# Performance work log

Hardware: AMD Instinct MI355X
Metric: run time of the kernel (lower is better)

## Reference

```python
import jax, jax.numpy as jnp
from jax import lax
import numpy as np


def gru_last(seq, Wih, Whh, bih, bhh):
    """Run a torch-style GRU over seq [N, T, C] and return only h_T [N, H].

    Gate order matches torch.nn.GRU: (r, z, n);
    n = tanh(W_in x + b_in + r * (W_hn h + b_hn)).
    """
    N = seq.shape[0]
    H = Whh.shape[1]

    def step(h, x_t):
        gi = x_t @ Wih.T + bih          # [N, 3H]
        gh = h @ Whh.T + bhh            # [N, 3H]
        i_r, i_z, i_n = jnp.split(gi, 3, axis=-1)
        h_r, h_z, h_n = jnp.split(gh, 3, axis=-1)
        r = jax.nn.sigmoid(i_r + h_r)
        z = jax.nn.sigmoid(i_z + h_z)
        n = jnp.tanh(i_n + r * h_n)
        h_new = (1.0 - z) * n + z * h
        return h_new, None

    h0 = jnp.zeros((N, H), dtype=seq.dtype)
    hT, _ = lax.scan(step, h0, jnp.swapaxes(seq, 0, 1))  # scan over T
    return hT


def setup_inputs() -> dict:
    key = jax.random.key(0)
    ks = jax.random.split(key, 12)
    B, C, T, Fq, H = 8, 64, 256, 256, 128
    s = 0.05
    return {
        "x": jax.random.normal(ks[0], (B, C, T, Fq), dtype=jnp.float32),
        "Wih_t": jax.random.normal(ks[1], (3 * H, C), dtype=jnp.float32) * s,
        "Whh_t": jax.random.normal(ks[2], (3 * H, H), dtype=jnp.float32) * s,
        "bih_t": jax.random.normal(ks[3], (3 * H,), dtype=jnp.float32) * s,
        "bhh_t": jax.random.normal(ks[4], (3 * H,), dtype=jnp.float32) * s,
        "Wih_f": jax.random.normal(ks[5], (3 * H, C), dtype=jnp.float32) * s,
        "Whh_f": jax.random.normal(ks[6], (3 * H, H), dtype=jnp.float32) * s,
        "bih_f": jax.random.normal(ks[7], (3 * H,), dtype=jnp.float32) * s,
        "bhh_f": jax.random.normal(ks[8], (3 * H,), dtype=jnp.float32) * s,
        "Wp": jax.random.normal(ks[9], (C, H), dtype=jnp.float32) * s,
        "bp": jax.random.normal(ks[10], (C,), dtype=jnp.float32) * s,
    }


def reference(x, Wih_t, Whh_t, bih_t, bhh_t, Wih_f, Whh_f, bih_f, bhh_f, Wp, bp):
    B, C, T, Fq = x.shape
    H = Whh_t.shape[1]

    # time GRU: sequences of length T, one per (batch, freq)
    t_in = jnp.transpose(x, (0, 3, 2, 1)).reshape(B * Fq, T, C)
    h_t = gru_last(t_in, Wih_t, Whh_t, bih_t, bhh_t)          # [B*F, H]
    t_vec = jnp.transpose(h_t.reshape(B, Fq, H), (0, 2, 1))    # [B, H, F]

    # freq GRU: sequences of length F, one per (batch, time)
    f_in = jnp.transpose(x, (0, 2, 3, 1)).reshape(B * T, Fq, C)
    h_f = gru_last(f_in, Wih_f, Whh_f, bih_f, bhh_f)          # [B*T, H]
    f_vec = jnp.transpose(h_f.reshape(B, T, H), (0, 2, 1))    # [B, H, T]

    # t_feat [B,H,F,1] expanded along dim2 to T (requires F == T),
    # f_feat [B,H,T,1] expanded along dim3 to F; fused is constant along F.
    s = t_vec + f_vec                                          # [B, H, T]  (F == T)
    out_t = jnp.einsum("ch,bht->bct", Wp, s) + bp[None, :, None]  # 1x1 conv
    return jnp.broadcast_to(out_t[:, :, :, None], (B, C, T, Fq))
```

## Files before the change

### kernel.cpp

```cpp
#include <hip/hip_runtime.h>

#define B_ 8
#define C_ 64
#define T_ 256
#define F_ 256
#define H_ 128
#define TF_ (T_*F_)

typedef _Float16 half_t;
typedef _Float16 half8 __attribute__((ext_vector_type(8)));
typedef float float4v __attribute__((ext_vector_type(4)));

#if __has_builtin(__builtin_amdgcn_exp2f)
#define EXP2F(x) __builtin_amdgcn_exp2f(x)
#else
static __device__ inline float EXP2F(float x) { float r; asm("v_exp_f32 %0, %1" : "=v"(r) : "v"(x)); return r; }
#endif
#if __has_builtin(__builtin_amdgcn_rcpf)
#define RCPF(x) __builtin_amdgcn_rcpf(x)
#else
static __device__ inline float RCPF(float x) { float r; asm("v_rcp_f32 %0, %1" : "=v"(r) : "v"(x)); return r; }
#endif

#define SGB __builtin_amdgcn_sched_group_barrier

#define NEG_L2E  (-1.4426950408889634f)
#define NEG_2L2E (-2.8853900817779268f)

__global__ __launch_bounds__(256) void k_transpose(const float* __restrict__ x,
                                                   half_t* __restrict__ xt) {
    __shared__ float lds[64 * 65];
    int blk = blockIdx.x;
    int b   = blk >> 10;
    int tf0 = (blk & 1023) << 6;
    int tid = threadIdx.x;
    int s = tid & 15;
    int q = tid >> 4;
    const float* xp = x + (size_t)(b * C_) * TF_ + tf0 + s * 4;
#pragma unroll
    for (int i = 0; i < 4; ++i) {
        int c = q + i * 16;
        float4v v = __builtin_nontemporal_load((const float4v*)(xp + (size_t)c * TF_));
#pragma unroll
        for (int j = 0; j < 4; ++j) lds[(s * 4 + j) * 65 + c] = v[j];
    }
    __syncthreads();
    int row = tid >> 2;
    int c0  = (tid & 3) << 4;
    float v[16];
#pragma unroll
    for (int k = 0; k < 16; ++k) v[k] = lds[row * 65 + c0 + k];
    half8 o0, o1;
#pragma unroll
    for (int k = 0; k < 8; ++k) { o0[k] = (half_t)v[k]; o1[k] = (half_t)v[8 + k]; }
    half_t* op = xt + ((size_t)b * TF_ + tf0 + row) * C_ + c0;
    *(half8*)op       = o0;
    *(half8*)(op + 8) = o1;
}

__device__ inline half8 load_w8s(const float* __restrict__ p, float s) {
    half8 r;
#pragma unroll
    for (int k = 0; k < 8; ++k) r[k] = (half_t)(p[k] * s);
    return r;
}

#define MFMA(a, b, c) __builtin_amdgcn_mfma_f32_16x16x32_f16((a), (b), (c), 0, 0, 0)

__global__ __launch_bounds__(512, 2) void k_gru(
    const half_t* __restrict__ xt,
    const float* __restrict__ Wih_t, const float* __restrict__ Whh_t,
    const float* __restrict__ bih_t, const float* __restrict__ bhh_t,
    const float* __restrict__ Wih_f, const float* __restrict__ Whh_f,
    const float* __restrict__ bih_f, const float* __restrict__ bhh_f,
    float* __restrict__ h_t_out, float* __restrict__ h_f_out) {
    __shared__ half_t hbuf0[16 * 136];
    __shared__ half_t hbuf1[16 * 136];

    int tid  = threadIdx.x;
    int w    = tid >> 6;
    int lane = tid & 63;
    int nidx = lane & 15;
    int quad = lane >> 4;

    int bi  = blockIdx.x;
    bool isf = bi >= 128;
    int lbi = bi & 127;
    int b   = lbi >> 4;
    int g16 = (lbi & 15) << 4;

    const float* Wih = isf ? Wih_f : Wih_t;
    const float* Whh = isf ? Whh_f : Whh_t;
    const float* bih = isf ? bih_f : bih_t;
    const float* bhh = isf ? bhh_f : bhh_t;
    float* hout      = isf ? h_f_out : h_t_out;

    size_t Sm = isf ? (size_t)(F_ * C_) : (size_t)C_;
    size_t Ss = isf ? (size_t)C_ : (size_t)(F_ * C_);
    size_t abase = (size_t)b * TF_ * C_ + (size_t)g16 * Sm;

    int gr = w * 16 + nidx;
    int gz = gr + 128;
    int gn = gr + 256;
    int ko = quad * 8;

    half8 wir0 = load_w8s(Wih + gr * 64 + ko,      NEG_L2E);
    half8 wir1 = load_w8s(Wih + gr * 64 + 32 + ko, NEG_L2E);
    half8 wiz0 = load_w8s(Wih + gz * 64 + ko,      NEG_L2E);
    half8 wiz1 = load_w8s(Wih + gz * 64 + 32 + ko, NEG_L2E);
    half8 win0 = load_w8s(Wih + gn * 64 + ko,      NEG_2L2E);
    half8 win1 = load_w8s(Wih + gn * 64 + 32 + ko, NEG_2L2E);
    half8 whr[4], whz[4], whn[4];
#pragma unroll
    for (int kt = 0; kt < 4; ++kt) {
        whr[kt] = load_w8s(Whh + gr * 128 + kt * 32 + ko, NEG_L2E);
        whz[kt] = load_w8s(Whh + gz * 128 + kt * 32 + ko, NEG_L2E);
        whn[kt] = load_w8s(Whh + gn * 128 + kt * 32 + ko, NEG_2L2E);
    }
    float br  = NEG_L2E  * (bih[gr] + bhh[gr]);
    float bz  = NEG_L2E  * (bih[gz] + bhh[gz]);
    float bin = NEG_2L2E * bih[gn];
    float bhn = NEG_2L2E * bhh[gn];
    float4v brv  = {br, br, br, br};
    float4v bzv  = {bz, bz, bz, bz};
    float4v bnv  = {bin, bin, bin, bin};
    float4v bhnv = {bhn, bhn, bhn, bhn};

    for (int idx = tid; idx < 16 * 136; idx += 512) hbuf0[idx] = (half_t)0.f;
    float h_old[4] = {0.f, 0.f, 0.f, 0.f};

    const half_t* ap = xt + abase + (size_t)nidx * Sm + ko;
    half8 xA0 = *(const half8*)ap;
    half8 xA1 = *(const half8*)(ap + 32);
    ap += Ss;
    half8 xB0 = *(const half8*)ap;
    half8 xB1 = *(const half8*)(ap + 32);
    ap += Ss;

    float4v xrE = MFMA(xA0, wir0, brv); xrE = MFMA(xA1, wir1, xrE);
    float4v xzE = MFMA(xA0, wiz0, bzv); xzE = MFMA(xA1, wiz1, xzE);
    float4v xnE = MFMA(xA0, win0, bnv); xnE = MFMA(xA1, win1, xnE);
    float4v xrO = {0.f, 0.f, 0.f, 0.f};
    float4v xzO = {0.f, 0.f, 0.f, 0.f};
    float4v xnO = {0.f, 0.f, 0.f, 0.f};
    __syncthreads();

#define GRU_STEP(RBUF, WBUF, XR, XZ, XN, XRn, XZn, XNn, XC0, XC1, XP0, XP1)     \
    {                                                                           \
        const half_t* hrow = (RBUF) + nidx * 136 + ko;                          \
        half8 ha0 = *(const half8*)(hrow);                                      \
        half8 ha1 = *(const half8*)(hrow + 32);                                 \
        half8 ha2 = *(const half8*)(hrow + 64);                                 \
        half8 ha3 = *(const half8*)(hrow + 96);                                 \
        XP0 = *(const half8*)ap;                                                \
        XP1 = *(const half8*)(ap + 32);                                         \
        ap += Ss;                                                               \
        XR = MFMA(ha0, whr[0], XR); XR = MFMA(ha1, whr[1], XR);                 \
        XR = MFMA(ha2, whr[2], XR); XR = MFMA(ha3, whr[3], XR);                 \
        XZ = MFMA(ha0, whz[0], XZ); XZ = MFMA(ha1, whz[1], XZ);                 \
        XZ = MFMA(ha2, whz[2], XZ); XZ = MFMA(ha3, whz[3], XZ);                 \
        float4v hnv = MFMA(ha0, whn[0], bhnv);                                  \
        hnv = MFMA(ha1, whn[1], hnv);                                           \
        float rr[4], Ez[4];                                                     \
        _Pragma("unroll")                                                       \
        for (int rg = 0; rg < 4; ++rg) rr[rg] = RCPF(1.f + EXP2F(XR[rg]));      \
        hnv = MFMA(ha2, whn[2], hnv);                                           \
        hnv = MFMA(ha3, whn[3], hnv);                                           \
        _Pragma("unroll")                                                       \
        for (int rg = 0; rg < 4; ++rg) Ez[rg] = EXP2F(XZ[rg]);                  \
                                          \
        XRn = MFMA(XC0, wir0, brv); XRn = MFMA(XC1, wir1, XRn);                 \
        XZn = MFMA(XC0, wiz0, bzv); XZn = MFMA(XC1, wiz1, XZn);                 \
        XNn = MFMA(XC0, win0, bnv); XNn = MFMA(XC1, win1, XNn);                 \
        _Pragma("unroll")                                                       \
        for (int rg = 0; rg < 4; ++rg) {                                        \
            float np  = XN[rg] + rr[rg] * hnv[rg];                              \
            float En  = EXP2F(np);                                              \
            float u   = __builtin_fmaf(h_old[rg], En, h_old[rg]);               \
            float t2  = u + Ez[rg];                                             \
            float num = __builtin_fmaf(-En, Ez[rg], t2);                        \
            float den = (1.f + En) * (1.f + Ez[rg]);                            \
            float h   = num * RCPF(den);                                        \
            h_old[rg] = h;                                                      \
            (WBUF)[(quad * 4 + rg) * 136 + w * 16 + nidx] = (half_t)h;          \
        }                                                                       \
                                     \
        SGB(0x100, 4, 0);                    \
        SGB(0x020, 2, 0);                    \
        SGB(0x008, 8, 0);                    \
        SGB(0x002, 12, 0);                   \
        SGB(0x008, 4, 0);                    \
        SGB(0x002, 8, 0);                    \
        SGB(0x008, 6, 0);                    \
        SGB(0x002, 48, 0);                   \
        SGB(0x200, 4, 0);                    \
        __syncthreads();                                                        \
    }

    for (int it = 0; it < 128; ++it) {
        GRU_STEP(hbuf0, hbuf1, xrE, xzE, xnE, xrO, xzO, xnO, xB0, xB1, xA0, xA1)
        GRU_STEP(hbuf1, hbuf0, xrO, xzO, xnO, xrE, xzE, xnE, xA0, xA1, xB0, xB1)
    }
#undef GRU_STEP

    int srow = (b << 8) + g16;
#pragma unroll
    for (int rg = 0; rg < 4; ++rg) {
        hout[(size_t)(srow + quad * 4 + rg) * H_ + w * 16 + nidx] = h_old[rg];
    }
}

__global__ __launch_bounds__(256) void k_out(const float* __restrict__ h_t,
                                             const float* __restrict__ h_f,
                                             const float* __restrict__ Wp,
                                             const float* __restrict__ bp,
                                             float* __restrict__ out) {
    __shared__ float sv[128];
    __shared__ float part[4][64];
    __shared__ float orow[64];
    int blk = blockIdx.x;
    int b = blk >> 8;
    int i = blk & 255;
    int tid = threadIdx.x;
    size_t hoff = ((size_t)(b * 256 + i)) * 128;
    if (tid < 128) sv[tid] = h_t[hoff + tid] + h_f[hoff + tid];
    __syncthreads();
    int c = tid & 63;
    int q = tid >> 6;
    float p = 0.f;
    const float* wp = Wp + c * 128 + q * 32;
#pragma unroll
    for (int k = 0; k < 32; ++k) p += wp[k] * sv[q * 32 + k];
    part[q][c] = p;
    __syncthreads();
    if (tid < 64) orow[tid] = part[0][tid] + part[1][tid] + part[2][tid] + part[3][tid] + bp[tid];
    __syncthreads();
    int wv   = tid >> 6;
    int lane = tid & 63;
#pragma unroll
    for (int itr = 0; itr < 16; ++itr) {
        int cc = itr * 4 + wv;
        float v = orow[cc];
        float4v vv = {v, v, v, v};
        __builtin_nontemporal_store(vv, (float4v*)(out + (((size_t)(b * 64 + cc)) * 256 + i) * 256 + lane * 4));
    }
}

extern "C" void kernel_launch(void* const* d_in, const int* in_sizes, int n_in,
                              void* d_out, int out_size, void* d_ws, size_t ws_size,
                              hipStream_t stream) {
    const float* x     = (const float*)d_in[0];
    const float* Wih_t = (const float*)d_in[1];
    const float* Whh_t = (const float*)d_in[2];
    const float* bih_t = (const float*)d_in[3];
    const float* bhh_t = (const float*)d_in[4];
    const float* Wih_f = (const float*)d_in[5];
    const float* Whh_f = (const float*)d_in[6];
    const float* bih_f = (const float*)d_in[7];
    const float* bhh_f = (const float*)d_in[8];
    const float* Wp    = (const float*)d_in[9];
    const float* bp    = (const float*)d_in[10];
    float* out = (float*)d_out;

    half_t* xt     = (half_t*)d_out;
    float* h_t_out = (float*)((char*)d_ws);
    float* h_f_out = (float*)((char*)d_ws + (size_t)2048 * 128 * 4);

    k_transpose<<<8192, 256, 0, stream>>>(x, xt);
    k_gru<<<256, 512, 0, stream>>>(xt, Wih_t, Whh_t, bih_t, bhh_t,
                                   Wih_f, Whh_f, bih_f, bhh_f, h_t_out, h_f_out);
    k_out<<<2048, 256, 0, stream>>>(h_t_out, h_f_out, Wp, bp, out);
}
```

Before: 433.7 us.

## Fuse input transpose into GRU kernel with strided fp32 loads

Removes the separate transpose/fp16-conversion kernel and has the GRU kernel read the original fp32 NCHW input directly, 16 scalar strided loads per lane per step, converting to half in registers. This eliminates a full read+write pass over the 128MB input and one launch, but replaces vectorized contiguous half8 loads with scattered scalar loads inside the serial recurrence, which may expose latency. The hand-tuned sched_group_barrier schedule is also dropped, and the loop is peeled to avoid out-of-range prefetch at the end.

```diff
diff --git a/kernel.cpp b/kernel.cpp
--- a/kernel.cpp
+++ b/kernel.cpp
@@ -22,42 +22,9 @@
 static __device__ inline float RCPF(float x) { float r; asm("v_rcp_f32 %0, %1" : "=v"(r) : "v"(x)); return r; }
 #endif
 
-#define SGB __builtin_amdgcn_sched_group_barrier
-
 #define NEG_L2E  (-1.4426950408889634f)
 #define NEG_2L2E (-2.8853900817779268f)
 
-__global__ __launch_bounds__(256) void k_transpose(const float* __restrict__ x,
-                                                   half_t* __restrict__ xt) {
-    __shared__ float lds[64 * 65];
-    int blk = blockIdx.x;
-    int b   = blk >> 10;
-    int tf0 = (blk & 1023) << 6;
-    int tid = threadIdx.x;
-    int s = tid & 15;
-    int q = tid >> 4;
-    const float* xp = x + (size_t)(b * C_) * TF_ + tf0 + s * 4;
-#pragma unroll
-    for (int i = 0; i < 4; ++i) {
-        int c = q + i * 16;
-        float4v v = __builtin_nontemporal_load((const float4v*)(xp + (size_t)c * TF_));
-#pragma unroll
-        for (int j = 0; j < 4; ++j) lds[(s * 4 + j) * 65 + c] = v[j];
-    }
-    __syncthreads();
-    int row = tid >> 2;
-    int c0  = (tid & 3) << 4;
-    float v[16];
-#pragma unroll
-    for (int k = 0; k < 16; ++k) v[k] = lds[row * 65 + c0 + k];
-    half8 o0, o1;
-#pragma unroll
-    for (int k = 0; k < 8; ++k) { o0[k] = (half_t)v[k]; o1[k] = (half_t)v[8 + k]; }
-    half_t* op = xt + ((size_t)b * TF_ + tf0 + row) * C_ + c0;
-    *(half8*)op       = o0;
-    *(half8*)(op + 8) = o1;
-}
-
 __device__ inline half8 load_w8s(const float* __restrict__ p, float s) {
     half8 r;
 #pragma unroll
@@ -68,7 +35,7 @@
 #define MFMA(a, b, c) __builtin_amdgcn_mfma_f32_16x16x32_f16((a), (b), (c), 0, 0, 0)
 
 __global__ __launch_bounds__(512, 2) void k_gru(
-    const half_t* __restrict__ xt,
+    const float* __restrict__ x,
     const float* __restrict__ Wih_t, const float* __restrict__ Whh_t,
     const float* __restrict__ bih_t, const float* __restrict__ bhh_t,
     const float* __restrict__ Wih_f, const float* __restrict__ Whh_f,
@@ -95,9 +62,21 @@
     const float* bhh = isf ? bhh_f : bhh_t;
     float* hout      = isf ? h_f_out : h_t_out;
 
-    size_t Sm = isf ? (size_t)(F_ * C_) : (size_t)C_;
-    size_t Ss = isf ? (size_t)C_ : (size_t)(F_ * C_);
-    size_t abase = (size_t)b * TF_ * C_ + (size_t)g16 * Sm;
+    int Lm = isf ? 256 : 1;
+    int As = isf ? 1 : 256;
+    const float* bp1 = x + (size_t)b * (64 * 65536) + (size_t)g16 * Lm;
+    const float* bp2 = bp1 + 32 * 65536;
+    int xoff = quad * 8 * 65536 + nidx * Lm;
+
+#define XLOAD(dst)                                                              \
+    {                                                                           \
+        _Pragma("unroll")                                                       \
+        for (int j = 0; j < 8; ++j) {                                           \
+            (dst)[j]     = bp1[xoff + j * 65536];                               \
+            (dst)[8 + j] = bp2[xoff + j * 65536];                               \
+        }                                                                       \
+        bp1 += As; bp2 += As;                                                   \
+    }
 
     int gr = w * 16 + nidx;
     int gz = gr + 128;
@@ -129,32 +108,29 @@
     for (int idx = tid; idx < 16 * 136; idx += 512) hbuf0[idx] = (half_t)0.f;
     float h_old[4] = {0.f, 0.f, 0.f, 0.f};
 
-    const half_t* ap = xt + abase + (size_t)nidx * Sm + ko;
-    half8 xA0 = *(const half8*)ap;
-    half8 xA1 = *(const half8*)(ap + 32);
-    ap += Ss;
-    half8 xB0 = *(const half8*)ap;
-    half8 xB1 = *(const half8*)(ap + 32);
-    ap += Ss;
-
-    float4v xrE = MFMA(xA0, wir0, brv); xrE = MFMA(xA1, wir1, xrE);
-    float4v xzE = MFMA(xA0, wiz0, bzv); xzE = MFMA(xA1, wiz1, xzE);
-    float4v xnE = MFMA(xA0, win0, bnv); xnE = MFMA(xA1, win1, xnE);
+    float xrawA[16], xrawB[16];
+    XLOAD(xrawA);
+    XLOAD(xrawB);
+
+    half8 a0, a1;
+#pragma unroll
+    for (int k2 = 0; k2 < 8; ++k2) { a0[k2] = (half_t)xrawA[k2]; a1[k2] = (half_t)xrawA[8 + k2]; }
+    float4v xrE = MFMA(a0, wir0, brv); xrE = MFMA(a1, wir1, xrE);
+    float4v xzE = MFMA(a0, wiz0, bzv); xzE = MFMA(a1, wiz1, xzE);
+    float4v xnE = MFMA(a0, win0, bnv); xnE = MFMA(a1, win1, xnE);
     float4v xrO = {0.f, 0.f, 0.f, 0.f};
     float4v xzO = {0.f, 0.f, 0.f, 0.f};
     float4v xnO = {0.f, 0.f, 0.f, 0.f};
     __syncthreads();
 
-#define GRU_STEP(RBUF, WBUF, XR, XZ, XN, XRn, XZn, XNn, XC0, XC1, XP0, XP1)     \
+#define GRU_STEP(RBUF, WBUF, XR, XZ, XN, XRn, XZn, XNn, XCraw, XPraw, PRE, REF) \
     {                                                                           \
         const half_t* hrow = (RBUF) + nidx * 136 + ko;                          \
         half8 ha0 = *(const half8*)(hrow);                                      \
         half8 ha1 = *(const half8*)(hrow + 32);                                 \
         half8 ha2 = *(const half8*)(hrow + 64);                                 \
         half8 ha3 = *(const half8*)(hrow + 96);                                 \
-        XP0 = *(const half8*)ap;                                                \
-        XP1 = *(const half8*)(ap + 32);                                         \
-        ap += Ss;                                                               \
+        if (PRE) { XLOAD(XPraw); }                                              \
         XR = MFMA(ha0, whr[0], XR); XR = MFMA(ha1, whr[1], XR);                 \
         XR = MFMA(ha2, whr[2], XR); XR = MFMA(ha3, whr[3], XR);                 \
         XZ = MFMA(ha0, whz[0], XZ); XZ = MFMA(ha1, whz[1], XZ);                 \
@@ -168,10 +144,17 @@
         hnv = MFMA(ha3, whn[3], hnv);                                           \
         _Pragma("unroll")                                                       \
         for (int rg = 0; rg < 4; ++rg) Ez[rg] = EXP2F(XZ[rg]);                  \
-                                          \
-        XRn = MFMA(XC0, wir0, brv); XRn = MFMA(XC1, wir1, XRn);                 \
-        XZn = MFMA(XC0, wiz0, bzv); XZn = MFMA(XC1, wiz1, XZn);                 \
-        XNn = MFMA(XC0, win0, bnv); XNn = MFMA(XC1, win1, XNn);                 \
+        if (REF) {                                                              \
+            half8 c0, c1;                                                       \
+            _Pragma("unroll")                                                   \
+            for (int k2 = 0; k2 < 8; ++k2) {                                    \
+                c0[k2] = (half_t)(XCraw)[k2];                                   \
+                c1[k2] = (half_t)(XCraw)[8 + k2];                               \
+            }                                                                   \
+            XRn = MFMA(c0, wir0, brv); XRn = MFMA(c1, wir1, XRn);               \
+            XZn = MFMA(c0, wiz0, bzv); XZn = MFMA(c1, wiz1, XZn);               \
+            XNn = MFMA(c0, win0, bnv); XNn = MFMA(c1, win1, XNn);               \
+        }                                                                       \
         _Pragma("unroll")                                                       \
         for (int rg = 0; rg < 4; ++rg) {                                        \
             float np  = XN[rg] + rr[rg] * hnv[rg];                              \
@@ -184,24 +167,17 @@
             h_old[rg] = h;                                                      \
             (WBUF)[(quad * 4 + rg) * 136 + w * 16 + nidx] = (half_t)h;          \
         }                                                                       \
-                                     \
-        SGB(0x100, 4, 0);                    \
-        SGB(0x020, 2, 0);                    \
-        SGB(0x008, 8, 0);                    \
-        SGB(0x002, 12, 0);                   \
-        SGB(0x008, 4, 0);                    \
-        SGB(0x002, 8, 0);                    \
-        SGB(0x008, 6, 0);                    \
-        SGB(0x002, 48, 0);                   \
-        SGB(0x200, 4, 0);                    \
         __syncthreads();                                                        \
     }
 
-    for (int it = 0; it < 128; ++it) {
-        GRU_STEP(hbuf0, hbuf1, xrE, xzE, xnE, xrO, xzO, xnO, xB0, xB1, xA0, xA1)
-        GRU_STEP(hbuf1, hbuf0, xrO, xzO, xnO, xrE, xzE, xnE, xA0, xA1, xB0, xB1)
-    }
+    for (int it = 0; it < 127; ++it) {
+        GRU_STEP(hbuf0, hbuf1, xrE, xzE, xnE, xrO, xzO, xnO, xrawB, xrawA, 1, 1)
+        GRU_STEP(hbuf1, hbuf0, xrO, xzO, xnO, xrE, xzE, xnE, xrawA, xrawB, 1, 1)
+    }
+    GRU_STEP(hbuf0, hbuf1, xrE, xzE, xnE, xrO, xzO, xnO, xrawB, xrawA, 0, 1)
+    GRU_STEP(hbuf1, hbuf0, xrO, xzO, xnO, xrE, xzE, xnE, xrawA, xrawB, 0, 0)
 #undef GRU_STEP
+#undef XLOAD
 
     int srow = (b << 8) + g16;
 #pragma unroll
@@ -262,12 +238,10 @@
     const float* bp    = (const float*)d_in[10];
     float* out = (float*)d_out;
 
-    half_t* xt     = (half_t*)d_out;
     float* h_t_out = (float*)((char*)d_ws);
     float* h_f_out = (float*)((char*)d_ws + (size_t)2048 * 128 * 4);
 
-    k_transpose<<<8192, 256, 0, stream>>>(x, xt);
-    k_gru<<<256, 512, 0, stream>>>(xt, Wih_t, Whh_t, bih_t, bhh_t,
+    k_gru<<<256, 512, 0, stream>>>(x, Wih_t, Whh_t, bih_t, bhh_t,
                                    Wih_f, Whh_f, bih_f, bhh_f, h_t_out, h_f_out);
     k_out<<<2048, 256, 0, stream>>>(h_t_out, h_f_out, Wp, bp, out);
 }
```

After: 1.244 ms. +186.9%, slower.
